# Optimization experiments

Hardware: AMD Instinct MI355X
Metric: run time of the kernel (lower is better)

The kernel has to match this reference:

```python
import jax, jax.numpy as jnp
import numpy as np

EPS = 1e-12
N_NODES = 100_000
E_UND = 1_600_000  # undirected edges; directed E = 2*E_UND
K = 8              # number of classes


def setup_inputs() -> dict:
    key = jax.random.key(0)
    k1, k2, k3, k4, k5 = jax.random.split(key, 5)
    # random undirected edges with no self-loops (u != v)
    u = jax.random.randint(k1, (E_UND,), 0, N_NODES, dtype=jnp.int32)
    off = jax.random.randint(k2, (E_UND,), 1, N_NODES, dtype=jnp.int32)
    v = ((u + off) % N_NODES).astype(jnp.int32)
    src = jnp.concatenate([u, v])
    dst = jnp.concatenate([v, u])
    # reverse-edge index: edge e=(src[e]->dst[e]) has reverse at rev_idx[e]
    rev_idx = jnp.concatenate([
        jnp.arange(E_UND, 2 * E_UND, dtype=jnp.int32),
        jnp.arange(E_UND, dtype=jnp.int32),
    ])
    prior = jax.random.uniform(k3, (N_NODES, K), dtype=jnp.float32)
    prior = prior / jnp.maximum(prior.sum(-1, keepdims=True), EPS)
    messages = jax.random.uniform(k4, (2 * E_UND, K), dtype=jnp.float32)
    messages = messages / jnp.maximum(messages.sum(-1, keepdims=True), EPS)
    potential = jax.random.uniform(k5, (K, K), dtype=jnp.float32)
    return {
        "prior": prior,
        "messages": messages,
        "potential": potential,
        "src": src,
        "dst": dst,
        "rev_idx": rev_idx,
        "iterations": 5,
    }


def reference(prior, messages, potential, src, dst, rev_idx, iterations):
    n = prior.shape[0]
    psi = jnp.exp(potential)  # [k,k]

    def step(msgs):
        # log of incoming messages, aggregated per destination node
        logm = jnp.log(jnp.maximum(msgs, EPS))                     # [E,k]
        in_log = jax.ops.segment_sum(logm, dst, num_segments=n)    # [n,k]
        # exclude-neighbor product for edge e=(i->j): all incoming to i
        # except the reverse message m[j->i]
        excl = jnp.exp(in_log[src] - logm[rev_idx])                # [E,k]
        b = jnp.maximum(prior[src] * excl, EPS)                    # [E,k]
        m_new = b @ psi                                            # [E,k]
        return m_new / jnp.maximum(m_new.sum(-1, keepdims=True), EPS)

    msgs = messages
    for _ in range(int(iterations)):  # synchronous BP updates, as in run_bp
        msgs = step(msgs)

    # beliefs: prior * product of ALL incoming messages, normalized
    in_log = jax.ops.segment_sum(jnp.log(jnp.maximum(msgs, EPS)), dst, num_segments=n)
    b = jnp.maximum(prior * jnp.exp(in_log), EPS)
    return b / jnp.maximum(b.sum(-1, keepdims=True), EPS)
```

## Files before the change

### kernel.cpp

```cpp
#include <hip/hip_runtime.h>
#include <hip/hip_fp16.h>

#define BP_EPS 1e-12f
#define BP_K 8
#define LOG_C 2.0f
#define CLAMP_SAFE -27.70f
#define THR_HOT    -27.80f
#define BSH 6
#define BNODES 64
#define NB1 512

typedef __attribute__((ext_vector_type(8))) _Float16 half8;


__global__ void k_hist(const int* __restrict__ src, const int* __restrict__ dst,
                       int* __restrict__ G, int Eu, int nbuck) {
    extern __shared__ int h[];
    for (int i = threadIdx.x; i < nbuck; i += blockDim.x) h[i] = 0;
    __syncthreads();
    int per = (Eu + NB1 - 1) / NB1;
    int s0 = blockIdx.x * per;
    int s1 = min(s0 + per, Eu);
    for (int e = s0 + threadIdx.x; e < s1; e += blockDim.x) {
        atomicAdd(&h[src[e] >> BSH], 1);
        atomicAdd(&h[dst[e] >> BSH], 1);
    }
    __syncthreads();
    for (int b = threadIdx.x; b < nbuck; b += blockDim.x)
        G[blockIdx.x * nbuck + b] = h[b];
}

__global__ void k_scanG(const int* __restrict__ G, int* __restrict__ Gpre,
                        int* __restrict__ total, int nbuck) {
    __shared__ int buf[NB1];
    int b = blockIdx.x;
    int t = threadIdx.x;
    int v = G[t * nbuck + b];
    buf[t] = v;
    __syncthreads();
    for (int off = 1; off < NB1; off <<= 1) {
        int x = (t >= off) ? buf[t - off] : 0;
        __syncthreads();
        buf[t] += x;
        __syncthreads();
    }
    Gpre[b * NB1 + t] = buf[t] - v;
    if (t == NB1 - 1) total[b] = buf[t];
}

__global__ void k_scanT(const int* __restrict__ total, int* __restrict__ base,
                        int nbuck, int* __restrict__ row_n, int E) {
    __shared__ int buf[1024];
    int t = threadIdx.x;
    int carry = 0;
    for (int s = 0; s < nbuck; s += 1024) {
        int i = s + t;
        int v = (i < nbuck) ? total[i] : 0;
        buf[t] = v;
        __syncthreads();
        for (int off = 1; off < 1024; off <<= 1) {
            int x = (t >= off) ? buf[t - off] : 0;
            __syncthreads();
            buf[t] += x;
            __syncthreads();
        }
        if (i < nbuck) base[i] = carry + buf[t] - v;
        carry += buf[1023];
        __syncthreads();
    }
    if (t == 0) { base[nbuck] = carry; *row_n = E; }
}

__global__ void k_scatter(const int* __restrict__ src, const int* __restrict__ dst,
                          const int* __restrict__ Gpre, const int* __restrict__ base,
                          int2* __restrict__ items, int Eu, int nbuck) {
    extern __shared__ int cur[];
    int blk = blockIdx.x;
    for (int i = threadIdx.x; i < nbuck; i += blockDim.x)
        cur[i] = base[i] + Gpre[i * NB1 + blk];
    __syncthreads();
    int per = (Eu + NB1 - 1) / NB1;
    int s0 = blk * per;
    int s1 = min(s0 + per, Eu);
    for (int e = s0 + threadIdx.x; e < s1; e += blockDim.x) {
        int u = src[e], v = dst[e];
        int pu = atomicAdd(&cur[u >> BSH], 1);
        items[pu] = make_int2(u, (e << 1) | 1);
        int pv = atomicAdd(&cur[v >> BSH], 1);
        items[pv] = make_int2(v, (e << 1) | 0);
    }
}

__global__ void k_csr(const int2* __restrict__ items, const int* __restrict__ base,
                      int* __restrict__ row, int* __restrict__ pos,
                      int* __restrict__ eid, int* __restrict__ nod, int n, int Eu) {
    __shared__ int deg[BNODES];
    __shared__ int cur[BNODES];
    int b = blockIdx.x;
    int lo = base[b], hi = base[b + 1];
    int node0 = b << BSH;
    if (threadIdx.x < BNODES) deg[threadIdx.x] = 0;
    __syncthreads();
    for (int i = lo + threadIdx.x; i < hi; i += blockDim.x)
        atomicAdd(&deg[items[i].x - node0], 1);
    __syncthreads();
    if (threadIdx.x == 0) {
        int acc = 0;
        for (int t = 0; t < BNODES; ++t) { int d = deg[t]; deg[t] = acc; acc += d; }
    }
    __syncthreads();
    if (threadIdx.x < BNODES) {
        int node = node0 + threadIdx.x;
        if (node < n) row[node] = lo + deg[threadIdx.x];
        cur[threadIdx.x] = deg[threadIdx.x];
    }
    __syncthreads();
    for (int i = lo + threadIdx.x; i < hi; i += blockDim.x) {
        int2 x = items[i];
        int p = atomicAdd(&cur[x.x - node0], 1);
        int slot = lo + p;
        pos[x.y] = slot;
        eid[slot] = (x.y >> 1) + (x.y & 1) * Eu;
        nod[slot] = x.x;
    }
}

__global__ void k_rev(const int* __restrict__ pos, int* __restrict__ rev, int Eu) {
    int e = blockIdx.x * blockDim.x + threadIdx.x;
    if (e < Eu) {
        int2 p = ((const int2*)pos)[e];
        rev[p.x] = p.y;
        rev[p.y] = p.x;
    }
}

__global__ void k_lp(const float* __restrict__ prior, float* __restrict__ LP, int n8) {
    int i = blockIdx.x * blockDim.x + threadIdx.x;
    if (i < n8) LP[i] = __logf(fmaxf(prior[i], BP_EPS));
}

__global__ void k_zero(int* __restrict__ nflag, unsigned int* __restrict__ bmap,
                       int* __restrict__ cnts, int n, int nb) {
    int i = blockIdx.x * blockDim.x + threadIdx.x;
    int st = gridDim.x * blockDim.x;
    for (int j = i; j < n; j += st) nflag[j] = 0;
    for (int j = i; j < nb; j += st) bmap[j] = 0;
    if (i < 16) cnts[i] = 0;
}

__device__ inline half8 bp_emit_bb(const float* bb, const float* psi) {
    float mn[BP_K];
    float sum = 0.0f;
#pragma unroll
    for (int jj = 0; jj < BP_K; ++jj) {
        float acc = 0.0f;
#pragma unroll
        for (int k = 0; k < BP_K; ++k) acc += bb[k] * psi[k * BP_K + jj];
        mn[jj] = acc;
        sum += acc;
    }
    float inv = 1.0f / fmaxf(sum, BP_EPS);
    half8 o;
#pragma unroll
    for (int jj = 0; jj < BP_K; ++jj)
        o[jj] = (_Float16)(__logf(fmaxf(mn[jj] * inv, BP_EPS)) + LOG_C);
    return o;
}

__device__ inline half8 bp_emit(const float* s, const float* lm, const float* psi) {
    float bb[BP_K];
#pragma unroll
    for (int k = 0; k < BP_K; ++k)
        bb[k] = fmaxf(__expf(s[k] - lm[k]), BP_EPS);
    return bp_emit_bb(bb, psi);
}

__device__ inline bool bp_allclamp(const float* s, const float* lm) {
    float m = s[0] - lm[0];
#pragma unroll
    for (int k = 1; k < BP_K; ++k) m = fmaxf(m, s[k] - lm[k]);
    return m < CLAMP_SAFE;
}

__device__ inline bool neq16(const void* oldp, const half8& v) {
    uint4 x = *(const uint4*)oldp;
    uint4 y;
    __builtin_memcpy(&y, &v, 16);
    return ((x.x ^ y.x) | (x.y ^ y.y) | (x.z ^ y.z) | (x.w ^ y.w)) != 0u;
}

#define INIT_PSI()                                                             \
    __shared__ float psi[BP_K * BP_K];                                         \
    if (threadIdx.x < BP_K * BP_K) psi[threadIdx.x] = expf(potential[threadIdx.x]); \
    __syncthreads();

#define INIT_WBAR()                                                            \
    __shared__ __align__(16) unsigned short wsh[8];                            \
    if (threadIdx.x == 0) {                                                    \
        float bbc[BP_K];                                                       \
        for (int k = 0; k < BP_K; ++k) bbc[k] = BP_EPS;                        \
        half8 wb = bp_emit_bb(bbc, psi);                                       \
        for (int k = 0; k < BP_K; ++k) wsh[k] = ((unsigned short*)&wb)[k];     \
    }                                                                          \
    __syncthreads();                                                           \
    half8 wbar = *(half8*)wsh;

__global__ void __launch_bounds__(256) k_fill(
        _Float16* __restrict__ Wex, const float* __restrict__ potential, int E) {
    INIT_PSI();
    INIT_WBAR();
    int st = gridDim.x * blockDim.x;
    for (int s = blockIdx.x * blockDim.x + threadIdx.x; s < E; s += st)
        *(half8*)(Wex + (size_t)s * BP_K) = wbar;
}

__global__ void __launch_bounds__(256) k_step1(
        const float* __restrict__ msgs, const int* __restrict__ eid,
        const int* __restrict__ row, const int* __restrict__ rev,
        const float* __restrict__ LP, const float* __restrict__ potential,
        _Float16* __restrict__ Wex, int* __restrict__ XS,
        unsigned int* __restrict__ bmap, int* __restrict__ cnts, int n) {
    INIT_PSI();

    int half = threadIdx.x >> 5;
    int sl = threadIdx.x & 31;
    int i = blockIdx.x * 8 + half;
    if (i >= n) return;

    int r0 = row[i];
    int r1 = row[i + 1];
    int j0 = r0 + sl;
    int j1 = j0 + 32;
    bool h0 = j0 < r1;
    bool h1 = j1 < r1;

    float s[BP_K];
#pragma unroll
    for (int k = 0; k < BP_K; ++k) s[k] = 0.0f;

    float lm0[BP_K], lm1[BP_K];

#define LOADF(J, LM)                                                          \
    {                                                                         \
        int id = eid[J];                                                      \
        const float4* m4 = (const float4*)(msgs + (size_t)id * BP_K);         \
        float4 x = m4[0], y = m4[1];                                          \
        float v[BP_K] = {x.x, x.y, x.z, x.w, y.x, y.y, y.z, y.w};             \
        _Pragma("unroll")                                                     \
        for (int k = 0; k < BP_K; ++k) LM[k] = __logf(fmaxf(v[k], BP_EPS));   \
    }

    if (h0) {
        LOADF(j0, lm0);
#pragma unroll
        for (int k = 0; k < BP_K; ++k) s[k] += lm0[k];
    }
    if (h1) {
        LOADF(j1, lm1);
#pragma unroll
        for (int k = 0; k < BP_K; ++k) s[k] += lm1[k];
    }
    for (int j = j0 + 64; j < r1; j += 32) {
        float t[BP_K];
        LOADF(j, t);
#pragma unroll
        for (int k = 0; k < BP_K; ++k) s[k] += t[k];
    }

#pragma unroll
    for (int off = 16; off >= 1; off >>= 1) {
#pragma unroll
        for (int k = 0; k < BP_K; ++k) s[k] += __shfl_xor(s[k], off);
    }
    {
        const float4* lp4 = (const float4*)(LP + (size_t)i * BP_K);
        float4 la = lp4[0], lb = lp4[1];
        s[0] += la.x; s[1] += la.y; s[2] += la.z; s[3] += la.w;
        s[4] += lb.x; s[5] += lb.y; s[6] += lb.z; s[7] += lb.w;
    }

#define EMIT1(J, LM)                                                          \
    if (!bp_allclamp(s, LM)) {                                                \
        int rv = rev[J];                                                      \
        *(half8*)(Wex + (size_t)rv * BP_K) = bp_emit(s, LM, psi);             \
        unsigned int mbit = 1u << (rv & 31);                                  \
        if (!(atomicOr(&bmap[rv >> 5], mbit) & mbit)) {                       \
            int idx = atomicAdd(&cnts[0], 1);                                 \
            XS[idx] = rv;                                                     \
        }                                                                     \
    }

    if (h0) EMIT1(j0, lm0)
    if (h1) EMIT1(j1, lm1)
    for (int j = j0 + 64; j < r1; j += 32) {
        float t[BP_K];
        LOADF(j, t);
        EMIT1(j, t)
    }
#undef EMIT1
#undef LOADF
}

__global__ void __launch_bounds__(256) k_mark(
        const int* __restrict__ row, const float* __restrict__ LP,
        const float* __restrict__ potential, const int* __restrict__ XS,
        const int* __restrict__ nod, const int* __restrict__ rev,
        int* __restrict__ nflag, int* __restrict__ Alist,
        int* __restrict__ cnts, int aidx, int n) {
    INIT_PSI();
    INIT_WBAR();
    float lw[BP_K];
#pragma unroll
    for (int k = 0; k < BP_K; ++k) lw[k] = (float)wbar[k] - LOG_C;

    int tid = blockIdx.x * blockDim.x + threadIdx.x;
    int st = gridDim.x * blockDim.x;

#define MARK(NODE)                                                            \
    {                                                                         \
        int nd_ = (NODE);                                                     \
        if (atomicExch(&nflag[nd_], 1) == 0) {                                \
            int ix = atomicAdd(&cnts[aidx], 1);                               \
            Alist[ix] = nd_;                                                  \
        }                                                                     \
    }

    for (int i = tid; i < n; i += st) {
        float dg = (float)(row[i + 1] - row[i]);
        const float4* lp4 = (const float4*)(LP + (size_t)i * BP_K);
        float4 la = lp4[0], lb = lp4[1];
        float lp[BP_K] = {la.x, la.y, la.z, la.w, lb.x, lb.y, lb.z, lb.w};
        float m = -1e30f;
#pragma unroll
        for (int k = 0; k < BP_K; ++k)
            m = fmaxf(m, dg * lw[k] + lp[k] - lw[k]);
        if (m >= THR_HOT) MARK(i)
    }
    int xc = cnts[0];
    for (int e = tid; e < xc; e += st) {
        int s = XS[e];
        MARK(nod[s])
        MARK(nod[rev[s]])
    }
#undef MARK
}

__global__ void __launch_bounds__(256) k_sparse(
        const _Float16* __restrict__ Wex, const int* __restrict__ row,
        const int* __restrict__ rev, const float* __restrict__ LP,
        const float* __restrict__ potential, const int* __restrict__ Alist,
        int* __restrict__ nflag, _Float16* __restrict__ Wst,
        int* __restrict__ Sslot, int* __restrict__ cnts, int aidx, int sidx) {
    INIT_PSI();
    INIT_WBAR();

    int half = threadIdx.x >> 5;
    int sl = threadIdx.x & 31;
    int cntA = cnts[aidx];

    for (int a = blockIdx.x * 8 + half; a < cntA; a += gridDim.x * 8) {
        int i = Alist[a];
        int r0 = row[i];
        int r1 = row[i + 1];

        float s[BP_K];
#pragma unroll
        for (int k = 0; k < BP_K; ++k) s[k] = 0.0f;

        for (int j = r0 + sl; j < r1; j += 32) {
            half8 h = *(const half8*)(Wex + (size_t)j * BP_K);
#pragma unroll
            for (int k = 0; k < BP_K; ++k) s[k] += (float)h[k] - LOG_C;
        }
#pragma unroll
        for (int off = 16; off >= 1; off >>= 1) {
#pragma unroll
            for (int k = 0; k < BP_K; ++k) s[k] += __shfl_xor(s[k], off);
        }
        {
            const float4* lp4 = (const float4*)(LP + (size_t)i * BP_K);
            float4 la = lp4[0], lb = lp4[1];
            s[0] += la.x; s[1] += la.y; s[2] += la.z; s[3] += la.w;
            s[4] += lb.x; s[5] += lb.y; s[6] += lb.z; s[7] += lb.w;
        }

        for (int j = r0 + sl; j < r1; j += 32) {
            half8 h = *(const half8*)(Wex + (size_t)j * BP_K);
            float lm[BP_K];
#pragma unroll
            for (int k = 0; k < BP_K; ++k) lm[k] = (float)h[k] - LOG_C;
            half8 nv = bp_allclamp(s, lm) ? wbar : bp_emit(s, lm, psi);
            int rv = rev[j];
            if (neq16(Wex + (size_t)rv * BP_K, nv)) {
                *(half8*)(Wst + (size_t)rv * BP_K) = nv;
                int idx = atomicAdd(&cnts[sidx], 1);
                Sslot[idx] = rv;
            }
        }
        if (sl == 0) nflag[i] = 0;
    }
}

__global__ void __launch_bounds__(256) k_apply(
        _Float16* __restrict__ Wex, const _Float16* __restrict__ Wst,
        const int* __restrict__ Sslot, int* __restrict__ XS,
        unsigned int* __restrict__ bmap, int* __restrict__ cnts, int sidx) {
    int cnt = cnts[sidx];
    int st = gridDim.x * blockDim.x;
    for (int e = blockIdx.x * blockDim.x + threadIdx.x; e < cnt; e += st) {
        int rv = Sslot[e];
        *(uint4*)(Wex + (size_t)rv * BP_K) = *(const uint4*)(Wst + (size_t)rv * BP_K);
        unsigned int mbit = 1u << (rv & 31);
        if (!(atomicOr(&bmap[rv >> 5], mbit) & mbit)) {
            int idx = atomicAdd(&cnts[0], 1);
            XS[idx] = rv;
        }
    }
}

__global__ void __launch_bounds__(256) k_belief(
        const _Float16* __restrict__ Wc, const int* __restrict__ row,
        const float* __restrict__ LP, float* __restrict__ out, int n) {
    int half = threadIdx.x >> 5;
    int sl = threadIdx.x & 31;
    int i = blockIdx.x * 8 + half;
    if (i >= n) return;

    int r0 = row[i];
    int r1 = row[i + 1];

    float s[BP_K];
#pragma unroll
    for (int k = 0; k < BP_K; ++k) s[k] = 0.0f;

    for (int j = r0 + sl; j < r1; j += 32) {
        half8 h = *(const half8*)(Wc + (size_t)j * BP_K);
#pragma unroll
        for (int k = 0; k < BP_K; ++k) s[k] += (float)h[k] - LOG_C;
    }

#pragma unroll
    for (int off = 16; off >= 1; off >>= 1) {
#pragma unroll
        for (int k = 0; k < BP_K; ++k) s[k] += __shfl_xor(s[k], off);
    }

    if (sl == 0) {
        const float4* lp4 = (const float4*)(LP + (size_t)i * BP_K);
        float4 la = lp4[0], lb = lp4[1];
        float lp[BP_K] = {la.x, la.y, la.z, la.w, lb.x, lb.y, lb.z, lb.w};
        float b[BP_K];
        float sum = 0.0f;
#pragma unroll
        for (int k = 0; k < BP_K; ++k) {
            b[k] = fmaxf(__expf(s[k] + lp[k]), BP_EPS);
            sum += b[k];
        }
        float inv = 1.0f / fmaxf(sum, BP_EPS);
        float4* o4 = (float4*)(out + (size_t)i * BP_K);
        o4[0] = {b[0] * inv, b[1] * inv, b[2] * inv, b[3] * inv};
        o4[1] = {b[4] * inv, b[5] * inv, b[6] * inv, b[7] * inv};
    }
}

extern "C" void kernel_launch(void* const* d_in, const int* in_sizes, int n_in,
                              void* d_out, int out_size, void* d_ws, size_t ws_size,
                              hipStream_t stream) {
    const float* prior     = (const float*)d_in[0];
    const float* msgs      = (const float*)d_in[1];
    const float* potential = (const float*)d_in[2];
    const int*   src       = (const int*)d_in[3];
    const int*   dst       = (const int*)d_in[4];
    const int ITERS = 5;

    int n  = in_sizes[0] / BP_K;
    int E  = in_sizes[3];
    int Eu = E / 2;
    int nbuck = (n + BNODES - 1) >> BSH;
    int nb32  = (E + 31) / 32;

    char* w = (char*)d_ws;
    _Float16* Wex = (_Float16*)w;  w += (size_t)E * 16;
    char*  R2     = w;             w += (size_t)E * 16;
    float* LP     = (float*)w;     w += (size_t)n * BP_K * sizeof(float);
    int*   G      = (int*)w;       w += (size_t)NB1 * nbuck * sizeof(int);
    int*   Gpre   = (int*)w;       w += (size_t)NB1 * nbuck * sizeof(int);
    int*   total  = (int*)w;       w += (size_t)nbuck * sizeof(int);
    int*   base   = (int*)w;       w += (size_t)(nbuck + 1) * sizeof(int);
    int*   row    = (int*)w;       w += (size_t)(n + 1) * sizeof(int);
    int*   rev    = (int*)w;       w += (size_t)E * sizeof(int);
    int*   nod    = (int*)w;       w += (size_t)E * sizeof(int);
    int*   XS     = (int*)w;       w += (size_t)E * sizeof(int);
    int*   Sslot  = (int*)w;       w += (size_t)E * sizeof(int);
    int*   Alist  = (int*)w;       w += (size_t)n * sizeof(int);
    int*   nflag  = (int*)w;       w += (size_t)n * sizeof(int);
    unsigned int* bmap = (unsigned int*)w; w += (size_t)nb32 * sizeof(unsigned int);
    int*   cnts   = (int*)w;       w += 16 * sizeof(int);
    int2*  items = (int2*)R2;
    int*   pos   = (int*)(R2 + (size_t)E * 8);
    int*   eid   = (int*)(R2 + (size_t)E * 12);
    _Float16* Wst = (_Float16*)R2;

    float* out = (float*)d_out;

    dim3 blk(256);
    dim3 grdEu((Eu + 255) / 256);
    dim3 grdNode((n + 7) / 8);
    size_t lds_hist = (size_t)nbuck * sizeof(int);

    k_hist   <<<NB1, blk, lds_hist, stream>>>(src, dst, G, Eu, nbuck);
    k_scanG  <<<nbuck, NB1, 0, stream>>>(G, Gpre, total, nbuck);
    k_scanT  <<<1, 1024, 0, stream>>>(total, base, nbuck, row + n, E);
    k_scatter<<<NB1, blk, lds_hist, stream>>>(src, dst, Gpre, base, items, Eu, nbuck);
    k_csr    <<<nbuck, blk, 0, stream>>>(items, base, row, pos, eid, nod, n, Eu);
    k_rev    <<<grdEu, blk, 0, stream>>>(pos, rev, Eu);
    k_lp     <<<(n * BP_K + 255) / 256, blk, 0, stream>>>(prior, LP, n * BP_K);
    k_zero   <<<512, blk, 0, stream>>>(nflag, bmap, cnts, n, nb32);
    k_fill   <<<1024, blk, 0, stream>>>(Wex, potential, E);

    k_step1<<<grdNode, blk, 0, stream>>>(msgs, eid, row, rev, LP, potential,
                                         Wex, XS, bmap, cnts, n);

    for (int t = 0; t < ITERS - 1; ++t) {
        int aidx = 1 + t;
        int sidx = 5 + t;
        k_mark  <<<512, blk, 0, stream>>>(row, LP, potential, XS, nod, rev,
                                          nflag, Alist, cnts, aidx, n);
        k_sparse<<<256, blk, 0, stream>>>(Wex, row, rev, LP, potential, Alist,
                                          nflag, Wst, Sslot, cnts, aidx, sidx);
        k_apply <<<256, blk, 0, stream>>>(Wex, Wst, Sslot, XS, bmap, cnts, sidx);
    }

    k_belief<<<grdNode, blk, 0, stream>>>(Wex, row, LP, out, n);
}
```

Before: 521.3 us.

## Drop dense Wex fill and rev build; gate reads by bitmap, sparse belief correction

Removes the k_fill kernel that wrote the default clamped message to all E slots, and the k_rev kernel. Reverse slots are now derived on the fly as pos[pay^1]. Reads of Wex in k_sparse are gated by the bitmap, falling back to the constant wbar for untouched slots. Staged updates are stored compactly (Sval indexed by list position) instead of in a dense E-sized staging array. The final belief pass becomes a per-node base (prior plus degree times default) plus atomic corrections over only the touched edges, avoiding a full sweep of Wex. The cost is extra indirection and bitmap lookups, plus float atomics in the belief stage.

```diff
diff --git a/kernel.cpp b/kernel.cpp
--- a/kernel.cpp
+++ b/kernel.cpp
@@ -93,7 +93,7 @@
 
 __global__ void k_csr(const int2* __restrict__ items, const int* __restrict__ base,
                       int* __restrict__ row, int* __restrict__ pos,
-                      int* __restrict__ eid, int* __restrict__ nod, int n, int Eu) {
+                      int* __restrict__ pay, int* __restrict__ nod, int n) {
     __shared__ int deg[BNODES];
     __shared__ int cur[BNODES];
     int b = blockIdx.x;
@@ -120,17 +120,8 @@
         int p = atomicAdd(&cur[x.x - node0], 1);
         int slot = lo + p;
         pos[x.y] = slot;
-        eid[slot] = (x.y >> 1) + (x.y & 1) * Eu;
+        pay[slot] = x.y;
         nod[slot] = x.x;
-    }
-}
-
-__global__ void k_rev(const int* __restrict__ pos, int* __restrict__ rev, int Eu) {
-    int e = blockIdx.x * blockDim.x + threadIdx.x;
-    if (e < Eu) {
-        int2 p = ((const int2*)pos)[e];
-        rev[p.x] = p.y;
-        rev[p.y] = p.x;
     }
 }
 
@@ -182,10 +173,10 @@
     return m < CLAMP_SAFE;
 }
 
-__device__ inline bool neq16(const void* oldp, const half8& v) {
-    uint4 x = *(const uint4*)oldp;
-    uint4 y;
-    __builtin_memcpy(&y, &v, 16);
+__device__ inline bool neq16(const half8& a, const half8& b) {
+    uint4 x, y;
+    __builtin_memcpy(&x, &a, 16);
+    __builtin_memcpy(&y, &b, 16);
     return ((x.x ^ y.x) | (x.y ^ y.y) | (x.z ^ y.z) | (x.w ^ y.w)) != 0u;
 }
 
@@ -205,21 +196,12 @@
     __syncthreads();                                                           \
     half8 wbar = *(half8*)wsh;
 
-__global__ void __launch_bounds__(256) k_fill(
-        _Float16* __restrict__ Wex, const float* __restrict__ potential, int E) {
-    INIT_PSI();
-    INIT_WBAR();
-    int st = gridDim.x * blockDim.x;
-    for (int s = blockIdx.x * blockDim.x + threadIdx.x; s < E; s += st)
-        *(half8*)(Wex + (size_t)s * BP_K) = wbar;
-}
-
 __global__ void __launch_bounds__(256) k_step1(
-        const float* __restrict__ msgs, const int* __restrict__ eid,
-        const int* __restrict__ row, const int* __restrict__ rev,
+        const float* __restrict__ msgs, const int* __restrict__ pay,
+        const int* __restrict__ pos, const int* __restrict__ row,
         const float* __restrict__ LP, const float* __restrict__ potential,
         _Float16* __restrict__ Wex, int* __restrict__ XS,
-        unsigned int* __restrict__ bmap, int* __restrict__ cnts, int n) {
+        unsigned int* __restrict__ bmap, int* __restrict__ cnts, int n, int Eu) {
     INIT_PSI();
 
     int half = threadIdx.x >> 5;
@@ -239,10 +221,12 @@
     for (int k = 0; k < BP_K; ++k) s[k] = 0.0f;
 
     float lm0[BP_K], lm1[BP_K];
-
-#define LOADF(J, LM)                                                          \
+    int py0 = 0, py1 = 0;
+
+#define LOADF(J, LM, PY)                                                      \
     {                                                                         \
-        int id = eid[J];                                                      \
+        PY = pay[J];                                                          \
+        int id = (PY >> 1) + (PY & 1) * Eu;                                   \
         const float4* m4 = (const float4*)(msgs + (size_t)id * BP_K);         \
         float4 x = m4[0], y = m4[1];                                          \
         float v[BP_K] = {x.x, x.y, x.z, x.w, y.x, y.y, y.z, y.w};             \
@@ -251,18 +235,19 @@
     }
 
     if (h0) {
-        LOADF(j0, lm0);
+        LOADF(j0, lm0, py0);
 #pragma unroll
         for (int k = 0; k < BP_K; ++k) s[k] += lm0[k];
     }
     if (h1) {
-        LOADF(j1, lm1);
+        LOADF(j1, lm1, py1);
 #pragma unroll
         for (int k = 0; k < BP_K; ++k) s[k] += lm1[k];
     }
     for (int j = j0 + 64; j < r1; j += 32) {
         float t[BP_K];
-        LOADF(j, t);
+        int pyt;
+        LOADF(j, t, pyt);
 #pragma unroll
         for (int k = 0; k < BP_K; ++k) s[k] += t[k];
     }
@@ -279,9 +264,9 @@
         s[4] += lb.x; s[5] += lb.y; s[6] += lb.z; s[7] += lb.w;
     }
 
-#define EMIT1(J, LM)                                                          \
+#define EMIT1(LM, PY)                                                         \
     if (!bp_allclamp(s, LM)) {                                                \
-        int rv = rev[J];                                                      \
+        int rv = pos[(PY) ^ 1];                                               \
         *(half8*)(Wex + (size_t)rv * BP_K) = bp_emit(s, LM, psi);             \
         unsigned int mbit = 1u << (rv & 31);                                  \
         if (!(atomicOr(&bmap[rv >> 5], mbit) & mbit)) {                       \
@@ -290,12 +275,13 @@
         }                                                                     \
     }
 
-    if (h0) EMIT1(j0, lm0)
-    if (h1) EMIT1(j1, lm1)
+    if (h0) EMIT1(lm0, py0)
+    if (h1) EMIT1(lm1, py1)
     for (int j = j0 + 64; j < r1; j += 32) {
         float t[BP_K];
-        LOADF(j, t);
-        EMIT1(j, t)
+        int pyt;
+        LOADF(j, t, pyt);
+        EMIT1(t, pyt)
     }
 #undef EMIT1
 #undef LOADF
@@ -304,9 +290,9 @@
 __global__ void __launch_bounds__(256) k_mark(
         const int* __restrict__ row, const float* __restrict__ LP,
         const float* __restrict__ potential, const int* __restrict__ XS,
-        const int* __restrict__ nod, const int* __restrict__ rev,
-        int* __restrict__ nflag, int* __restrict__ Alist,
-        int* __restrict__ cnts, int aidx, int n) {
+        const int* __restrict__ nod, const int* __restrict__ pay,
+        const int* __restrict__ pos, int* __restrict__ nflag,
+        int* __restrict__ Alist, int* __restrict__ cnts, int aidx, int n) {
     INIT_PSI();
     INIT_WBAR();
     float lw[BP_K];
@@ -340,23 +326,31 @@
     for (int e = tid; e < xc; e += st) {
         int s = XS[e];
         MARK(nod[s])
-        MARK(nod[rev[s]])
+        MARK(nod[pos[pay[s] ^ 1]])
     }
 #undef MARK
 }
 
 __global__ void __launch_bounds__(256) k_sparse(
         const _Float16* __restrict__ Wex, const int* __restrict__ row,
-        const int* __restrict__ rev, const float* __restrict__ LP,
+        const int* __restrict__ pay, const int* __restrict__ pos,
+        const unsigned int* __restrict__ bmap, const float* __restrict__ LP,
         const float* __restrict__ potential, const int* __restrict__ Alist,
-        int* __restrict__ nflag, _Float16* __restrict__ Wst,
-        int* __restrict__ Sslot, int* __restrict__ cnts, int aidx, int sidx) {
+        int* __restrict__ nflag, int* __restrict__ Sslot,
+        _Float16* __restrict__ Sval, int* __restrict__ cnts, int aidx, int sidx) {
     INIT_PSI();
     INIT_WBAR();
 
     int half = threadIdx.x >> 5;
     int sl = threadIdx.x & 31;
     int cntA = cnts[aidx];
+
+#define GATED(J, H)                                                           \
+    half8 H;                                                                  \
+    {                                                                         \
+        bool ex_ = (bmap[(J) >> 5] >> ((J) & 31)) & 1;                        \
+        H = ex_ ? *(const half8*)(Wex + (size_t)(J) * BP_K) : wbar;           \
+    }
 
     for (int a = blockIdx.x * 8 + half; a < cntA; a += gridDim.x * 8) {
         int i = Alist[a];
@@ -368,7 +362,7 @@
         for (int k = 0; k < BP_K; ++k) s[k] = 0.0f;
 
         for (int j = r0 + sl; j < r1; j += 32) {
-            half8 h = *(const half8*)(Wex + (size_t)j * BP_K);
+            GATED(j, h)
 #pragma unroll
             for (int k = 0; k < BP_K; ++k) s[k] += (float)h[k] - LOG_C;
         }
@@ -385,31 +379,33 @@
         }
 
         for (int j = r0 + sl; j < r1; j += 32) {
-            half8 h = *(const half8*)(Wex + (size_t)j * BP_K);
+            GATED(j, h)
             float lm[BP_K];
 #pragma unroll
             for (int k = 0; k < BP_K; ++k) lm[k] = (float)h[k] - LOG_C;
             half8 nv = bp_allclamp(s, lm) ? wbar : bp_emit(s, lm, psi);
-            int rv = rev[j];
-            if (neq16(Wex + (size_t)rv * BP_K, nv)) {
-                *(half8*)(Wst + (size_t)rv * BP_K) = nv;
+            int rv = pos[pay[j] ^ 1];
+            GATED(rv, cv)
+            if (neq16(cv, nv)) {
                 int idx = atomicAdd(&cnts[sidx], 1);
                 Sslot[idx] = rv;
+                *(half8*)(Sval + (size_t)idx * BP_K) = nv;
             }
         }
         if (sl == 0) nflag[i] = 0;
     }
+#undef GATED
 }
 
 __global__ void __launch_bounds__(256) k_apply(
-        _Float16* __restrict__ Wex, const _Float16* __restrict__ Wst,
-        const int* __restrict__ Sslot, int* __restrict__ XS,
+        _Float16* __restrict__ Wex, const int* __restrict__ Sslot,
+        const _Float16* __restrict__ Sval, int* __restrict__ XS,
         unsigned int* __restrict__ bmap, int* __restrict__ cnts, int sidx) {
     int cnt = cnts[sidx];
     int st = gridDim.x * blockDim.x;
     for (int e = blockIdx.x * blockDim.x + threadIdx.x; e < cnt; e += st) {
         int rv = Sslot[e];
-        *(uint4*)(Wex + (size_t)rv * BP_K) = *(const uint4*)(Wst + (size_t)rv * BP_K);
+        *(half8*)(Wex + (size_t)rv * BP_K) = *(const half8*)(Sval + (size_t)e * BP_K);
         unsigned int mbit = 1u << (rv & 31);
         if (!(atomicOr(&bmap[rv >> 5], mbit) & mbit)) {
             int idx = atomicAdd(&cnts[0], 1);
@@ -418,42 +414,61 @@
     }
 }
 
-__global__ void __launch_bounds__(256) k_belief(
-        const _Float16* __restrict__ Wc, const int* __restrict__ row,
-        const float* __restrict__ LP, float* __restrict__ out, int n) {
-    int half = threadIdx.x >> 5;
-    int sl = threadIdx.x & 31;
-    int i = blockIdx.x * 8 + half;
-    if (i >= n) return;
-
-    int r0 = row[i];
-    int r1 = row[i + 1];
-
-    float s[BP_K];
-#pragma unroll
-    for (int k = 0; k < BP_K; ++k) s[k] = 0.0f;
-
-    for (int j = r0 + sl; j < r1; j += 32) {
-        half8 h = *(const half8*)(Wc + (size_t)j * BP_K);
-#pragma unroll
-        for (int k = 0; k < BP_K; ++k) s[k] += (float)h[k] - LOG_C;
-    }
-
-#pragma unroll
-    for (int off = 16; off >= 1; off >>= 1) {
-#pragma unroll
-        for (int k = 0; k < BP_K; ++k) s[k] += __shfl_xor(s[k], off);
-    }
-
-    if (sl == 0) {
+__global__ void __launch_bounds__(256) kb_base(
+        const int* __restrict__ row, const float* __restrict__ LP,
+        const float* __restrict__ potential, float* __restrict__ BA, int n) {
+    INIT_PSI();
+    INIT_WBAR();
+    float lw[BP_K];
+#pragma unroll
+    for (int k = 0; k < BP_K; ++k) lw[k] = (float)wbar[k] - LOG_C;
+    int st = gridDim.x * blockDim.x;
+    for (int i = blockIdx.x * blockDim.x + threadIdx.x; i < n; i += st) {
+        float dg = (float)(row[i + 1] - row[i]);
         const float4* lp4 = (const float4*)(LP + (size_t)i * BP_K);
         float4 la = lp4[0], lb = lp4[1];
         float lp[BP_K] = {la.x, la.y, la.z, la.w, lb.x, lb.y, lb.z, lb.w};
+        float4* o4 = (float4*)(BA + (size_t)i * BP_K);
+        o4[0] = {lp[0] + dg * lw[0], lp[1] + dg * lw[1],
+                 lp[2] + dg * lw[2], lp[3] + dg * lw[3]};
+        o4[1] = {lp[4] + dg * lw[4], lp[5] + dg * lw[5],
+                 lp[6] + dg * lw[6], lp[7] + dg * lw[7]};
+    }
+}
+
+__global__ void __launch_bounds__(256) kb_corr(
+        const _Float16* __restrict__ Wex, const int* __restrict__ XS,
+        const int* __restrict__ nod, const float* __restrict__ potential,
+        float* __restrict__ BA, const int* __restrict__ cnts) {
+    INIT_PSI();
+    INIT_WBAR();
+    float lw[BP_K];
+#pragma unroll
+    for (int k = 0; k < BP_K; ++k) lw[k] = (float)wbar[k] - LOG_C;
+    int cnt = cnts[0];
+    int st = gridDim.x * blockDim.x;
+    for (int e = blockIdx.x * blockDim.x + threadIdx.x; e < cnt; e += st) {
+        int s = XS[e];
+        int i = nod[s];
+        half8 h = *(const half8*)(Wex + (size_t)s * BP_K);
+#pragma unroll
+        for (int k = 0; k < BP_K; ++k)
+            atomicAdd(&BA[(size_t)i * BP_K + k], ((float)h[k] - LOG_C) - lw[k]);
+    }
+}
+
+__global__ void __launch_bounds__(256) kb_norm(
+        const float* __restrict__ BA, float* __restrict__ out, int n) {
+    int st = gridDim.x * blockDim.x;
+    for (int i = blockIdx.x * blockDim.x + threadIdx.x; i < n; i += st) {
+        const float4* s4 = (const float4*)(BA + (size_t)i * BP_K);
+        float4 sa = s4[0], sb = s4[1];
+        float s[BP_K] = {sa.x, sa.y, sa.z, sa.w, sb.x, sb.y, sb.z, sb.w};
         float b[BP_K];
         float sum = 0.0f;
 #pragma unroll
         for (int k = 0; k < BP_K; ++k) {
-            b[k] = fmaxf(__expf(s[k] + lp[k]), BP_EPS);
+            b[k] = fmaxf(__expf(s[k]), BP_EPS);
             sum += b[k];
         }
         float inv = 1.0f / fmaxf(sum, BP_EPS);
@@ -481,25 +496,24 @@
 
     char* w = (char*)d_ws;
     _Float16* Wex = (_Float16*)w;  w += (size_t)E * 16;
-    char*  R2     = w;             w += (size_t)E * 16;
+    int2*  items  = (int2*)w;      w += (size_t)E * sizeof(int2);
+    int*   pos    = (int*)w;       w += (size_t)E * sizeof(int);
+    int*   pay    = (int*)w;       w += (size_t)E * sizeof(int);
+    int*   nod    = (int*)w;       w += (size_t)E * sizeof(int);
+    int*   XS     = (int*)w;       w += (size_t)E * sizeof(int);
+    int*   Sslot  = (int*)w;       w += (size_t)Eu * sizeof(int);
+    _Float16* Sval = (_Float16*)w; w += (size_t)Eu * 16;
     float* LP     = (float*)w;     w += (size_t)n * BP_K * sizeof(float);
+    float* BA     = (float*)w;     w += (size_t)n * BP_K * sizeof(float);
     int*   G      = (int*)w;       w += (size_t)NB1 * nbuck * sizeof(int);
     int*   Gpre   = (int*)w;       w += (size_t)NB1 * nbuck * sizeof(int);
     int*   total  = (int*)w;       w += (size_t)nbuck * sizeof(int);
     int*   base   = (int*)w;       w += (size_t)(nbuck + 1) * sizeof(int);
     int*   row    = (int*)w;       w += (size_t)(n + 1) * sizeof(int);
-    int*   rev    = (int*)w;       w += (size_t)E * sizeof(int);
-    int*   nod    = (int*)w;       w += (size_t)E * sizeof(int);
-    int*   XS     = (int*)w;       w += (size_t)E * sizeof(int);
-    int*   Sslot  = (int*)w;       w += (size_t)E * sizeof(int);
     int*   Alist  = (int*)w;       w += (size_t)n * sizeof(int);
     int*   nflag  = (int*)w;       w += (size_t)n * sizeof(int);
     unsigned int* bmap = (unsigned int*)w; w += (size_t)nb32 * sizeof(unsigned int);
     int*   cnts   = (int*)w;       w += 16 * sizeof(int);
-    int2*  items = (int2*)R2;
-    int*   pos   = (int*)(R2 + (size_t)E * 8);
-    int*   eid   = (int*)(R2 + (size_t)E * 12);
-    _Float16* Wst = (_Float16*)R2;
 
     float* out = (float*)d_out;
 
@@ -512,24 +526,25 @@
     k_scanG  <<<nbuck, NB1, 0, stream>>>(G, Gpre, total, nbuck);
     k_scanT  <<<1, 1024, 0, stream>>>(total, base, nbuck, row + n, E);
     k_scatter<<<NB1, blk, lds_hist, stream>>>(src, dst, Gpre, base, items, Eu, nbuck);
-    k_csr    <<<nbuck, blk, 0, stream>>>(items, base, row, pos, eid, nod, n, Eu);
-    k_rev    <<<grdEu, blk, 0, stream>>>(pos, rev, Eu);
+    k_csr    <<<nbuck, blk, 0, stream>>>(items, base, row, pos, pay, nod, n);
     k_lp     <<<(n * BP_K + 255) / 256, blk, 0, stream>>>(prior, LP, n * BP_K);
     k_zero   <<<512, blk, 0, stream>>>(nflag, bmap, cnts, n, nb32);
-    k_fill   <<<1024, blk, 0, stream>>>(Wex, potential, E);
-
-    k_step1<<<grdNode, blk, 0, stream>>>(msgs, eid, row, rev, LP, potential,
-                                         Wex, XS, bmap, cnts, n);
+
+    k_step1<<<grdNode, blk, 0, stream>>>(msgs, pay, pos, row, LP, potential,
+                                         Wex, XS, bmap, cnts, n, Eu);
 
     for (int t = 0; t < ITERS - 1; ++t) {
         int aidx = 1 + t;
         int sidx = 5 + t;
-        k_mark  <<<512, blk, 0, stream>>>(row, LP, potential, XS, nod, rev,
+        k_mark  <<<512, blk, 0, stream>>>(row, LP, potential, XS, nod, pay, pos,
                                           nflag, Alist, cnts, aidx, n);
-        k_sparse<<<256, blk, 0, stream>>>(Wex, row, rev, LP, potential, Alist,
-                                          nflag, Wst, Sslot, cnts, aidx, sidx);
-        k_apply <<<256, blk, 0, stream>>>(Wex, Wst, Sslot, XS, bmap, cnts, sidx);
-    }
-
-    k_belief<<<grdNode, blk, 0, stream>>>(Wex, row, LP, out, n);
-}
+        k_sparse<<<256, blk, 0, stream>>>(Wex, row, pay, pos, bmap, LP, potential,
+                                          Alist, nflag, Sslot, Sval, cnts,
+                                          aidx, sidx);
+        k_apply <<<256, blk, 0, stream>>>(Wex, Sslot, Sval, XS, bmap, cnts, sidx);
+    }
+
+    kb_base<<<512, blk, 0, stream>>>(row, LP, potential, BA, n);
+    kb_corr<<<256, blk, 0, stream>>>(Wex, XS, nod, potential, BA, cnts);
+    kb_norm<<<512, blk, 0, stream>>>(BA, out, n);
+}
```

Result: faster. 464.8 us (-10.8%).
